# Kernel tuning notes

Hardware: AMD Instinct MI355X
Metric: run time of the kernel (lower is better)

Reference implementation:

```python
import jax, jax.numpy as jnp
import numpy as np

B, C, H, W = 256, 3, 84, 84
HID, VOCAB = 768, 50257
INPUT_DIM = H * W
EPS = 1e-8


def setup_inputs() -> dict:
    key = jax.random.key(0)
    k1, k2, k3 = jax.random.split(key, 3)
    observations = jax.random.normal(k1, (B, C, H, W), dtype=jnp.float32)
    word_embs = jax.random.normal(k2, (VOCAB, HID), dtype=jnp.float32)
    # torch.normal(mean=0, std=1/sqrt(hidden_dim), size=(hidden_dim, input_dim))
    rand_obs_proj = jax.random.normal(k3, (HID, INPUT_DIM), dtype=jnp.float32) / np.sqrt(HID)
    return {"observations": observations, "word_embs": word_embs,
            "rand_obs_proj": rand_obs_proj, "beta": 8}


def reference(observations, word_embs, rand_obs_proj, beta):
    # _preprocess_obs: mean over channel dim, then flatten each sample
    obs = observations.mean(axis=1).reshape(observations.shape[0], -1)  # [B, H*W]
    q = obs @ rand_obs_proj.T                                           # [B, HID]
    q_norm = jnp.linalg.norm(q, axis=-1, keepdims=True)                 # [B, 1]
    e_norm = jnp.linalg.norm(word_embs, axis=-1)[None, :]               # [1, V]
    sims = (q @ word_embs.T) / (q_norm * e_norm + EPS)                  # [B, V]
    softm = jax.nn.softmax(beta * sims, axis=-1)
    state = softm @ word_embs                                           # [B, HID]
    return state
```

## Files before the change

### kernel.cpp

```cpp
#include <hip/hip_runtime.h>


#define VOCAB 50257
#define VPAD  50304
#define HID   768
#define BATCH 256
#define IN    7056
#define INPAD 7072
#define NPAIR (INPAD / 2)
#define SPLITS 32
#define CHUNK 1600
#define QSPLITS 17
#define QCHUNK 416

typedef __attribute__((ext_vector_type(8))) __bf16 bf16x8;
typedef __attribute__((ext_vector_type(4))) float f32x4;

__device__ inline unsigned short f2bf(float f) {
  union { float f; unsigned u; } v; v.f = f;
  unsigned r = v.u + 0x7fffu + ((v.u >> 16) & 1u);
  return (unsigned short)(r >> 16);
}
__device__ inline unsigned pack2(float lo, float hi) {
  return (unsigned)f2bf(lo) | ((unsigned)f2bf(hi) << 16);
}

__global__ __launch_bounds__(256, 3) void k_wprep(const float* __restrict__ W,
                                                  unsigned* __restrict__ Wb,
                                                  float* __restrict__ inv_en) {
  __shared__ float ssb[32][8];
  const int t = threadIdx.x;
  const int lane = t & 63, wave = t >> 6;
  const int v0 = blockIdx.x * 32;

  float4 xv[8][3];
#pragma unroll
  for (int rr = 0; rr < 8; rr++) {
    const int v = v0 + wave * 8 + rr;
    const int vc = (v < VOCAB) ? v : (VOCAB - 1);
    const float* wrow = &W[(size_t)vc * HID + lane * 4];
#pragma unroll
    for (int c = 0; c < 3; c++)
      xv[rr][c] = *(const float4*)(wrow + c * 256);
  }
  __builtin_amdgcn_sched_barrier(0);
#pragma unroll
  for (int rr = 0; rr < 8; rr++) {
    const int row = wave * 8 + rr;
    const int v = v0 + row;
    const bool valid = (v < VOCAB);
    unsigned* wbrow = &Wb[(size_t)v * (HID / 2) + lane * 2];
    float ss = 0.f;
#pragma unroll
    for (int c = 0; c < 3; c++) {
      float4 x = xv[rr][c];
      if (!valid) x = (float4){0.f, 0.f, 0.f, 0.f};
      *(uint2*)&wbrow[c * 128] = (uint2){pack2(x.x, x.y), pack2(x.z, x.w)};
      ss += x.x * x.x + x.y * x.y + x.z * x.z + x.w * x.w;
    }
    ss += __shfl_xor(ss, 1, 64);
    ss += __shfl_xor(ss, 2, 64);
    ss += __shfl_xor(ss, 4, 64);
    if ((lane & 7) == 0) ssb[row][lane >> 3] = ss;
  }
  __syncthreads();
  {
    const int row = t >> 3, j = t & 7;
    float s = ssb[row][j];
    s += __shfl_xor(s, 1, 64);
    s += __shfl_xor(s, 2, 64);
    s += __shfl_xor(s, 4, 64);
    if (j == 0) {
      const int v = v0 + row;
      inv_en[v] = (v < VOCAB) ? (1.f / sqrtf(s)) : 0.f;
    }
  }
}

__global__ __launch_bounds__(256) void k_obs(const float* __restrict__ obs,
                                             unsigned* __restrict__ obsb) {
  int b = blockIdx.x, t = threadIdx.x;
  const size_t base = (size_t)b * 3 * IN;
  for (int p = t; p < NPAIR; p += 256) {
    float x = 0.f, y = 0.f;
    if (2 * p < IN) {
      float2 a0 = *(const float2*)&obs[base + 2 * p];
      float2 a1 = *(const float2*)&obs[base + IN + 2 * p];
      float2 a2 = *(const float2*)&obs[base + 2 * IN + 2 * p];
      x = (a0.x + a1.x + a2.x) * (1.f / 3.f);
      y = (a0.y + a1.y + a2.y) * (1.f / 3.f);
    }
    obsb[b * NPAIR + p] = pack2(x, y);
  }
}

__global__ __launch_bounds__(256) void k_proj(const float* __restrict__ proj,
                                              unsigned* __restrict__ projb) {
  int h = blockIdx.x, t = threadIdx.x;
  for (int p = t; p < NPAIR; p += 256) {
    float x = 0.f, y = 0.f;
    if (2 * p < IN) {
      float2 xy = *(const float2*)&proj[(size_t)h * IN + 2 * p];
      x = xy.x; y = xy.y;
    }
    projb[h * NPAIR + p] = pack2(x, y);
  }
}


__global__ __launch_bounds__(256) void k_qgemm(const unsigned short* __restrict__ A,
                                               const unsigned short* __restrict__ Bm,
                                               float* __restrict__ qp) {
  __shared__ unsigned short As[64][32];
  __shared__ unsigned short Bs[64][32];
  const int t = threadIdx.x;
  const int lane = t & 63, wave = t >> 6;
  const int wm = wave >> 1, wn = wave & 1;
  const int quad = lane >> 4, lo = lane & 15;
  const int m0 = blockIdx.y * 64, n0 = blockIdx.x * 64;
  const int split = blockIdx.z;
  const int kbeg = split * QCHUNK, kend = kbeg + QCHUNK;
  const int ar = t >> 2, ac = (t & 3) * 8;
  f32x4 acc[2][2];
  for (int i = 0; i < 2; i++)
    for (int j = 0; j < 2; j++) acc[i][j] = (f32x4){0.f, 0.f, 0.f, 0.f};
  const unsigned short* aptr = &A[(m0 + ar) * INPAD + ac];
  const unsigned short* bptr = &Bm[(n0 + ar) * INPAD + ac];
  for (int k0 = kbeg; k0 < kend; k0 += 32) {
    uint4 av = *(const uint4*)(aptr + k0);
    uint4 bv = *(const uint4*)(bptr + k0);
    __syncthreads();
    *(uint4*)&As[ar][ac] = av;
    *(uint4*)&Bs[ar][ac] = bv;
    __syncthreads();
    bf16x8 af[2], bfr[2];
    for (int i = 0; i < 2; i++) {
      af[i]  = *(const bf16x8*)&As[wm * 32 + i * 16 + lo][quad * 8];
      bfr[i] = *(const bf16x8*)&Bs[wn * 32 + i * 16 + lo][quad * 8];
    }
    for (int mi = 0; mi < 2; mi++)
      for (int ni = 0; ni < 2; ni++)
        acc[mi][ni] = __builtin_amdgcn_mfma_f32_16x16x32_bf16(af[mi], bfr[ni], acc[mi][ni], 0, 0, 0);
  }
  float* outp = qp + (size_t)split * BATCH * HID;
  for (int mi = 0; mi < 2; mi++)
    for (int ni = 0; ni < 2; ni++)
      for (int r = 0; r < 4; r++) {
        int row = m0 + wm * 32 + mi * 16 + quad * 4 + r;
        int col = n0 + wn * 32 + ni * 16 + lo;
        outp[row * HID + col] = acc[mi][ni][r];
      }
}

__global__ __launch_bounds__(384) void k_qhat(const float* __restrict__ qp,
                                              const int* __restrict__ beta,
                                              unsigned* __restrict__ qhat,
                                              float* __restrict__ l) {
  int b = blockIdx.x, t = threadIdx.x;
  float x = 0.f, y = 0.f;
  for (int s = 0; s < QSPLITS; s++) {
    float2 p = *(const float2*)&qp[(size_t)s * BATCH * HID + b * HID + 2 * t];
    x += p.x; y += p.y;
  }
  float ss = x * x + y * y;
  for (int m = 1; m < 64; m <<= 1) ss += __shfl_xor(ss, m, 64);
  __shared__ float sacc[6];
  if ((t & 63) == 0) sacc[t >> 6] = ss;
  __syncthreads();
  float tot = sacc[0] + sacc[1] + sacc[2] + sacc[3] + sacc[4] + sacc[5];
  float scale = (float)beta[0] / sqrtf(tot);
  qhat[b * (HID / 2) + t] = pack2(x * scale, y * scale);
  if (t == 0) l[b] = 0.f;
}


__global__ __launch_bounds__(256) void k_gemm1(const unsigned short* __restrict__ A,
                                               const unsigned short* __restrict__ Bm,
                                               const float* __restrict__ inv_en,
                                               unsigned short* __restrict__ E,
                                               float* __restrict__ l) {
  __shared__ unsigned short As[128][32];
  __shared__ unsigned short Bs[128][32];
  __shared__ unsigned short Et[128][128];
  __shared__ float rowsum[128];
  const int t = threadIdx.x;
  const int lane = t & 63, wave = t >> 6;
  const int wm = wave >> 1, wn = wave & 1;
  const int quad = lane >> 4, lo = lane & 15;
  const int m0 = blockIdx.x * 128, n0 = blockIdx.y * 128;
  const int ar = t >> 2, ac = (t & 3) * 8;
  if (t < 128) rowsum[t] = 0.f;
  f32x4 acc[4][4];
  for (int i = 0; i < 4; i++)
    for (int j = 0; j < 4; j++) acc[i][j] = (f32x4){0.f, 0.f, 0.f, 0.f};
  const unsigned short* aptr  = &A[(m0 + ar) * HID + ac];
  const unsigned short* aptr2 = &A[(m0 + ar + 64) * HID + ac];
  const unsigned short* bptr  = &Bm[(size_t)(n0 + ar) * HID + ac];
  const unsigned short* bptr2 = &Bm[(size_t)(n0 + ar + 64) * HID + ac];
  uint4 av0 = *(const uint4*)(aptr);
  uint4 av1 = *(const uint4*)(aptr2);
  uint4 bv0 = *(const uint4*)(bptr);
  uint4 bv1 = *(const uint4*)(bptr2);
  for (int k0 = 0; k0 < HID; k0 += 32) {
    __syncthreads();
    *(uint4*)&As[ar][ac]      = av0;
    *(uint4*)&As[ar + 64][ac] = av1;
    *(uint4*)&Bs[ar][ac]      = bv0;
    *(uint4*)&Bs[ar + 64][ac] = bv1;
    __syncthreads();
    const int kn = (k0 + 32 < HID) ? k0 + 32 : 0;
    av0 = *(const uint4*)(aptr + kn);
    av1 = *(const uint4*)(aptr2 + kn);
    bv0 = *(const uint4*)(bptr + kn);
    bv1 = *(const uint4*)(bptr2 + kn);
    __builtin_amdgcn_sched_barrier(0);
    bf16x8 af[4], bfr[4];
    for (int i = 0; i < 4; i++) {
      af[i]  = *(const bf16x8*)&As[wm * 64 + i * 16 + lo][quad * 8];
      bfr[i] = *(const bf16x8*)&Bs[wn * 64 + i * 16 + lo][quad * 8];
    }
    for (int mi = 0; mi < 4; mi++)
      for (int ni = 0; ni < 4; ni++)
        acc[mi][ni] = __builtin_amdgcn_mfma_f32_16x16x32_bf16(af[mi], bfr[ni], acc[mi][ni], 0, 0, 0);
  }
  for (int mi = 0; mi < 4; mi++)
    for (int ni = 0; ni < 4; ni++) {
      int cl = wn * 64 + ni * 16 + lo;
      int vg = n0 + cl;
      bool valid = (vg < VOCAB);
      float ie = inv_en[vg];
      for (int r = 0; r < 4; r++) {
        int row = wm * 64 + mi * 16 + quad * 4 + r;
        float e = valid ? __expf(acc[mi][ni][r] * ie) : 0.f;
        Et[row][cl] = f2bf(e);
        float s = e;
        s += __shfl_xor(s, 1, 64);
        s += __shfl_xor(s, 2, 64);
        s += __shfl_xor(s, 4, 64);
        s += __shfl_xor(s, 8, 64);
        if (lo == 0) atomicAdd(&rowsum[row], s);
      }
    }
  __syncthreads();
  for (int i = 0; i < 8; i++) {
    int idx = t + i * 256;
    int row = idx >> 4, j = idx & 15;
    *(uint4*)&E[(size_t)(m0 + row) * VPAD + n0 + j * 8] = *(const uint4*)&Et[row][j * 8];
  }
  if (t < 128) atomicAdd(&l[m0 + t], rowsum[t]);
}


__global__ __launch_bounds__(256) void k_gemm2(const unsigned short* __restrict__ Wb,
                                               const unsigned short* __restrict__ Bm,
                                               float* __restrict__ Pp) {
  __shared__ unsigned short As[128][34];
  __shared__ unsigned short Bs[128][32];
  const int t = threadIdx.x;
  const int lane = t & 63, wave = t >> 6;
  const int wm = wave >> 1, wn = wave & 1;
  const int quad = lane >> 4, lo = lane & 15;
  const int m0 = blockIdx.x * 128, n0 = blockIdx.y * 128;
  const int split = blockIdx.z;
  const int kbeg = split * CHUNK;
  const int kend = (kbeg + CHUNK < VPAD) ? kbeg + CHUNK : VPAD;
  const int sv = t >> 3, shc = t & 7;
  const int ar = t >> 2, ac = (t & 3) * 8;
  f32x4 acc[4][4];
  for (int i = 0; i < 4; i++)
    for (int j = 0; j < 4; j++) acc[i][j] = (f32x4){0.f, 0.f, 0.f, 0.f};
  const unsigned short* bptr  = &Bm[(size_t)(n0 + ar) * VPAD + ac];
  const unsigned short* bptr2 = &Bm[(size_t)(n0 + ar + 64) * VPAD + ac];
  uint4 a0  = *(const uint4*)&Wb[(size_t)(kbeg + sv) * HID + m0 + shc * 8];
  uint4 a1  = *(const uint4*)&Wb[(size_t)(kbeg + sv) * HID + m0 + (shc + 8) * 8];
  uint4 bv0 = *(const uint4*)(bptr + kbeg);
  uint4 bv1 = *(const uint4*)(bptr2 + kbeg);
  for (int k0 = kbeg; k0 < kend; k0 += 32) {
    __syncthreads();
    {
      const unsigned short* e0 = (const unsigned short*)&a0;
      const unsigned short* e1 = (const unsigned short*)&a1;
#pragma unroll
      for (int j = 0; j < 8; j++) {
        As[shc * 8 + j][sv]       = e0[j];
        As[(shc + 8) * 8 + j][sv] = e1[j];
      }
    }
    *(uint4*)&Bs[ar][ac]      = bv0;
    *(uint4*)&Bs[ar + 64][ac] = bv1;
    __syncthreads();
    const int kn = (k0 + 32 < kend) ? k0 + 32 : kbeg;
    a0  = *(const uint4*)&Wb[(size_t)(kn + sv) * HID + m0 + shc * 8];
    a1  = *(const uint4*)&Wb[(size_t)(kn + sv) * HID + m0 + (shc + 8) * 8];
    bv0 = *(const uint4*)(bptr + kn);
    bv1 = *(const uint4*)(bptr2 + kn);
    __builtin_amdgcn_sched_barrier(0);
    bf16x8 af[4], bfr[4];
#pragma unroll
    for (int i = 0; i < 4; i++) {
      const unsigned* rp = (const unsigned*)&As[wm * 64 + i * 16 + lo][quad * 8];
      uint4 u; u.x = rp[0]; u.y = rp[1]; u.z = rp[2]; u.w = rp[3];
      af[i]  = *(const bf16x8*)&u;
      bfr[i] = *(const bf16x8*)&Bs[wn * 64 + i * 16 + lo][quad * 8];
    }
    for (int mi = 0; mi < 4; mi++)
      for (int ni = 0; ni < 4; ni++)
        acc[mi][ni] = __builtin_amdgcn_mfma_f32_16x16x32_bf16(af[mi], bfr[ni], acc[mi][ni], 0, 0, 0);
  }
  float* outp = Pp + (size_t)split * HID * BATCH;
  for (int mi = 0; mi < 4; mi++)
    for (int ni = 0; ni < 4; ni++)
      for (int r = 0; r < 4; r++) {
        int h = m0 + wm * 64 + mi * 16 + quad * 4 + r;
        int b = n0 + wn * 64 + ni * 16 + lo;
        outp[h * BATCH + b] = acc[mi][ni][r];
      }
}

__global__ __launch_bounds__(256) void k_reduce(const float* __restrict__ Pp,
                                                const float* __restrict__ l,
                                                float* __restrict__ out) {
  int idx = blockIdx.x * 256 + threadIdx.x;
  int h = idx >> 8, b = idx & 255;
  float s = 0.f;
  for (int i = 0; i < SPLITS; i++) s += Pp[(size_t)i * (HID * BATCH) + idx];
  out[b * HID + h] = s / l[b];
}


extern "C" void kernel_launch(void* const* d_in, const int* in_sizes, int n_in,
                              void* d_out, int out_size, void* d_ws, size_t ws_size,
                              hipStream_t stream) {
  const float* obs  = (const float*)d_in[0];
  const float* W    = (const float*)d_in[1];
  const float* proj = (const float*)d_in[2];
  const int* beta   = (const int*)d_in[3];
  float* out = (float*)d_out;

  char* ws = (char*)d_ws;
  size_t off = 0;
  auto alloc = [&](size_t bytes) -> void* {
    void* p = ws + off;
    off = (off + bytes + 255) & ~(size_t)255;
    return p;
  };
  unsigned short* Wb    = (unsigned short*)alloc((size_t)VPAD * HID * 2);
  float* inv_en         = (float*)alloc((size_t)VPAD * 4);
  unsigned short* obsb  = (unsigned short*)alloc((size_t)BATCH * INPAD * 2);
  unsigned short* projb = (unsigned short*)alloc((size_t)HID * INPAD * 2);
  unsigned short* qhat  = (unsigned short*)alloc((size_t)BATCH * HID * 2);
  float* l              = (float*)alloc((size_t)BATCH * 4);
  unsigned short* E     = (unsigned short*)alloc((size_t)BATCH * VPAD * 2);
  float* Pp             = (float*)alloc((size_t)SPLITS * BATCH * HID * 4);
  float* qp             = Pp;
  (void)ws_size; (void)in_sizes; (void)n_in; (void)out_size;

  k_wprep<<<dim3(VPAD / 32), dim3(256), 0, stream>>>(W, (unsigned*)Wb, inv_en);
  k_obs  <<<dim3(BATCH), dim3(256), 0, stream>>>(obs, (unsigned*)obsb);
  k_proj <<<dim3(HID), dim3(256), 0, stream>>>(proj, (unsigned*)projb);
  k_qgemm<<<dim3(HID / 64, BATCH / 64, QSPLITS), dim3(256), 0, stream>>>(obsb, projb, qp);
  k_qhat <<<dim3(BATCH), dim3(384), 0, stream>>>(qp, beta, (unsigned*)qhat, l);
  k_gemm1<<<dim3(BATCH / 128, VPAD / 128), dim3(256), 0, stream>>>(qhat, Wb, inv_en, E, l);
  k_gemm2<<<dim3(HID / 128, BATCH / 128, SPLITS), dim3(256), 0, stream>>>(Wb, E, Pp);
  k_reduce<<<dim3(BATCH * HID / 256), dim3(256), 0, stream>>>(Pp, l, out);
}
```

Before: 406.2 us.

## Fuse word-embedding bf16 conversion and norm computation into the similarity GEMM

Removes the separate k_wprep pass. k_gemm1 now loads fp32 embeddings directly, converts them to bf16 for the MFMA tiles, and accumulates per-row sums of squares to get inverse norms locally. Blocks with blockIdx.x==0 also write the bf16 copy that k_gemm2 still needs. This saves one kernel launch and one full read of the fp32 table. In exchange, gemm1 reads fp32 data (twice the bytes of the bf16 path) in both of its M blocks, and does the conversion work redundantly.

After: 412.5 us. About the same (+1.5%).

```diff
diff --git a/kernel.cpp b/kernel.cpp
--- a/kernel.cpp
+++ b/kernel.cpp
@@ -23,58 +23,6 @@
 }
 __device__ inline unsigned pack2(float lo, float hi) {
   return (unsigned)f2bf(lo) | ((unsigned)f2bf(hi) << 16);
-}
-
-__global__ __launch_bounds__(256, 3) void k_wprep(const float* __restrict__ W,
-                                                  unsigned* __restrict__ Wb,
-                                                  float* __restrict__ inv_en) {
-  __shared__ float ssb[32][8];
-  const int t = threadIdx.x;
-  const int lane = t & 63, wave = t >> 6;
-  const int v0 = blockIdx.x * 32;
-
-  float4 xv[8][3];
-#pragma unroll
-  for (int rr = 0; rr < 8; rr++) {
-    const int v = v0 + wave * 8 + rr;
-    const int vc = (v < VOCAB) ? v : (VOCAB - 1);
-    const float* wrow = &W[(size_t)vc * HID + lane * 4];
-#pragma unroll
-    for (int c = 0; c < 3; c++)
-      xv[rr][c] = *(const float4*)(wrow + c * 256);
-  }
-  __builtin_amdgcn_sched_barrier(0);
-#pragma unroll
-  for (int rr = 0; rr < 8; rr++) {
-    const int row = wave * 8 + rr;
-    const int v = v0 + row;
-    const bool valid = (v < VOCAB);
-    unsigned* wbrow = &Wb[(size_t)v * (HID / 2) + lane * 2];
-    float ss = 0.f;
-#pragma unroll
-    for (int c = 0; c < 3; c++) {
-      float4 x = xv[rr][c];
-      if (!valid) x = (float4){0.f, 0.f, 0.f, 0.f};
-      *(uint2*)&wbrow[c * 128] = (uint2){pack2(x.x, x.y), pack2(x.z, x.w)};
-      ss += x.x * x.x + x.y * x.y + x.z * x.z + x.w * x.w;
-    }
-    ss += __shfl_xor(ss, 1, 64);
-    ss += __shfl_xor(ss, 2, 64);
-    ss += __shfl_xor(ss, 4, 64);
-    if ((lane & 7) == 0) ssb[row][lane >> 3] = ss;
-  }
-  __syncthreads();
-  {
-    const int row = t >> 3, j = t & 7;
-    float s = ssb[row][j];
-    s += __shfl_xor(s, 1, 64);
-    s += __shfl_xor(s, 2, 64);
-    s += __shfl_xor(s, 4, 64);
-    if (j == 0) {
-      const int v = v0 + row;
-      inv_en[v] = (v < VOCAB) ? (1.f / sqrtf(s)) : 0.f;
-    }
-  }
 }
 
 __global__ __launch_bounds__(256) void k_obs(const float* __restrict__ obs,
@@ -175,44 +123,66 @@
 
 
 __global__ __launch_bounds__(256) void k_gemm1(const unsigned short* __restrict__ A,
-                                               const unsigned short* __restrict__ Bm,
-                                               const float* __restrict__ inv_en,
+                                               const float* __restrict__ Wf,
+                                               unsigned* __restrict__ Wb,
                                                unsigned short* __restrict__ E,
                                                float* __restrict__ l) {
   __shared__ unsigned short As[128][32];
   __shared__ unsigned short Bs[128][32];
   __shared__ unsigned short Et[128][128];
   __shared__ float rowsum[128];
+  __shared__ float inv_l[128];
   const int t = threadIdx.x;
   const int lane = t & 63, wave = t >> 6;
   const int wm = wave >> 1, wn = wave & 1;
   const int quad = lane >> 4, lo = lane & 15;
   const int m0 = blockIdx.x * 128, n0 = blockIdx.y * 128;
   const int ar = t >> 2, ac = (t & 3) * 8;
+  const bool bx0 = (blockIdx.x == 0);
   if (t < 128) rowsum[t] = 0.f;
   f32x4 acc[4][4];
   for (int i = 0; i < 4; i++)
     for (int j = 0; j < 4; j++) acc[i][j] = (f32x4){0.f, 0.f, 0.f, 0.f};
   const unsigned short* aptr  = &A[(m0 + ar) * HID + ac];
   const unsigned short* aptr2 = &A[(m0 + ar + 64) * HID + ac];
-  const unsigned short* bptr  = &Bm[(size_t)(n0 + ar) * HID + ac];
-  const unsigned short* bptr2 = &Bm[(size_t)(n0 + ar + 64) * HID + ac];
-  uint4 av0 = *(const uint4*)(aptr);
-  uint4 av1 = *(const uint4*)(aptr2);
-  uint4 bv0 = *(const uint4*)(bptr);
-  uint4 bv1 = *(const uint4*)(bptr2);
+  const int vr0 = n0 + ar, vr1 = n0 + ar + 64;
+  const int vc0 = (vr0 < VOCAB) ? vr0 : (VOCAB - 1);
+  const int vc1 = (vr1 < VOCAB) ? vr1 : (VOCAB - 1);
+  const float* wp0 = &Wf[(size_t)vc0 * HID + ac];
+  const float* wp1 = &Wf[(size_t)vc1 * HID + ac];
+  float ss0 = 0.f, ss1 = 0.f;
+  uint4 av0  = *(const uint4*)(aptr);
+  uint4 av1  = *(const uint4*)(aptr2);
+  float4 b0a = *(const float4*)(wp0);
+  float4 b0b = *(const float4*)(wp0 + 4);
+  float4 b1a = *(const float4*)(wp1);
+  float4 b1b = *(const float4*)(wp1 + 4);
   for (int k0 = 0; k0 < HID; k0 += 32) {
     __syncthreads();
     *(uint4*)&As[ar][ac]      = av0;
     *(uint4*)&As[ar + 64][ac] = av1;
-    *(uint4*)&Bs[ar][ac]      = bv0;
-    *(uint4*)&Bs[ar + 64][ac] = bv1;
+    uint4 w0 = (uint4){pack2(b0a.x, b0a.y), pack2(b0a.z, b0a.w),
+                       pack2(b0b.x, b0b.y), pack2(b0b.z, b0b.w)};
+    uint4 w1 = (uint4){pack2(b1a.x, b1a.y), pack2(b1a.z, b1a.w),
+                       pack2(b1b.x, b1b.y), pack2(b1b.z, b1b.w)};
+    *(uint4*)&Bs[ar][ac]      = w0;
+    *(uint4*)&Bs[ar + 64][ac] = w1;
+    ss0 += b0a.x * b0a.x + b0a.y * b0a.y + b0a.z * b0a.z + b0a.w * b0a.w
+         + b0b.x * b0b.x + b0b.y * b0b.y + b0b.z * b0b.z + b0b.w * b0b.w;
+    ss1 += b1a.x * b1a.x + b1a.y * b1a.y + b1a.z * b1a.z + b1a.w * b1a.w
+         + b1b.x * b1b.x + b1b.y * b1b.y + b1b.z * b1b.z + b1b.w * b1b.w;
+    if (bx0) {
+      *(uint4*)&Wb[(size_t)vr0 * (HID / 2) + (k0 + ac) / 2] = w0;
+      *(uint4*)&Wb[(size_t)vr1 * (HID / 2) + (k0 + ac) / 2] = w1;
+    }
     __syncthreads();
     const int kn = (k0 + 32 < HID) ? k0 + 32 : 0;
     av0 = *(const uint4*)(aptr + kn);
     av1 = *(const uint4*)(aptr2 + kn);
-    bv0 = *(const uint4*)(bptr + kn);
-    bv1 = *(const uint4*)(bptr2 + kn);
+    b0a = *(const float4*)(wp0 + kn);
+    b0b = *(const float4*)(wp0 + kn + 4);
+    b1a = *(const float4*)(wp1 + kn);
+    b1b = *(const float4*)(wp1 + kn + 4);
     __builtin_amdgcn_sched_barrier(0);
     bf16x8 af[4], bfr[4];
     for (int i = 0; i < 4; i++) {
@@ -223,12 +193,21 @@
       for (int ni = 0; ni < 4; ni++)
         acc[mi][ni] = __builtin_amdgcn_mfma_f32_16x16x32_bf16(af[mi], bfr[ni], acc[mi][ni], 0, 0, 0);
   }
+  ss0 += __shfl_xor(ss0, 1, 64);
+  ss0 += __shfl_xor(ss0, 2, 64);
+  ss1 += __shfl_xor(ss1, 1, 64);
+  ss1 += __shfl_xor(ss1, 2, 64);
+  if ((t & 3) == 0) {
+    inv_l[ar]      = (vr0 < VOCAB) ? (1.f / sqrtf(ss0)) : 0.f;
+    inv_l[ar + 64] = (vr1 < VOCAB) ? (1.f / sqrtf(ss1)) : 0.f;
+  }
+  __syncthreads();
   for (int mi = 0; mi < 4; mi++)
     for (int ni = 0; ni < 4; ni++) {
       int cl = wn * 64 + ni * 16 + lo;
       int vg = n0 + cl;
       bool valid = (vg < VOCAB);
-      float ie = inv_en[vg];
+      float ie = inv_l[cl];
       for (int r = 0; r < 4; r++) {
         int row = wm * 64 + mi * 16 + quad * 4 + r;
         float e = valid ? __expf(acc[mi][ni][r] * ie) : 0.f;
@@ -345,7 +324,6 @@
     return p;
   };
   unsigned short* Wb    = (unsigned short*)alloc((size_t)VPAD * HID * 2);
-  float* inv_en         = (float*)alloc((size_t)VPAD * 4);
   unsigned short* obsb  = (unsigned short*)alloc((size_t)BATCH * INPAD * 2);
   unsigned short* projb = (unsigned short*)alloc((size_t)HID * INPAD * 2);
   unsigned short* qhat  = (unsigned short*)alloc((size_t)BATCH * HID * 2);
@@ -355,12 +333,11 @@
   float* qp             = Pp;
   (void)ws_size; (void)in_sizes; (void)n_in; (void)out_size;
 
-  k_wprep<<<dim3(VPAD / 32), dim3(256), 0, stream>>>(W, (unsigned*)Wb, inv_en);
   k_obs  <<<dim3(BATCH), dim3(256), 0, stream>>>(obs, (unsigned*)obsb);
   k_proj <<<dim3(HID), dim3(256), 0, stream>>>(proj, (unsigned*)projb);
   k_qgemm<<<dim3(HID / 64, BATCH / 64, QSPLITS), dim3(256), 0, stream>>>(obsb, projb, qp);
   k_qhat <<<dim3(BATCH), dim3(384), 0, stream>>>(qp, beta, (unsigned*)qhat, l);
-  k_gemm1<<<dim3(BATCH / 128, VPAD / 128), dim3(256), 0, stream>>>(qhat, Wb, inv_en, E, l);
+  k_gemm1<<<dim3(BATCH / 128, VPAD / 128), dim3(256), 0, stream>>>(qhat, W, (unsigned*)Wb, E, l);
   k_gemm2<<<dim3(HID / 128, BATCH / 128, SPLITS), dim3(256), 0, stream>>>(Wb, E, Pp);
   k_reduce<<<dim3(BATCH * HID / 256), dim3(256), 0, stream>>>(Pp, l, out);
 }
```
